# Kernel tuning notes

Measured on AMD Instinct MI355X. Metric: run time of the kernel, lower is better.

Reference implementation:

```python
import jax, jax.numpy as jnp
import numpy as np

N_NODES = 250000
N_EDGES = 4000000

def gcn_layer(x, src, dst, W, b, n_nodes):
    # PyG GCNConv: linear transform, add self-loops, symmetric normalization,
    # scatter-add aggregation at target nodes, then bias.
    xw = x @ W                                            # [N, out]
    deg = jax.ops.segment_sum(jnp.ones_like(src, dtype=xw.dtype), dst,
                              num_segments=n_nodes) + 1.0  # +1 for self loop
    dinv = deg ** -0.5                                     # deg >= 1 due to self loops
    norm = dinv[src] * dinv[dst]                           # [E]
    agg = jax.ops.segment_sum(norm[:, None] * xw[src], dst,
                              num_segments=n_nodes)        # neighbor messages
    out = agg + (dinv * dinv)[:, None] * xw + b            # self-loop message + bias
    return out


def setup_inputs() -> dict:
    key = jax.random.key(0)
    ks = jax.random.split(key, 8)
    x = jax.random.normal(ks[0], (N_NODES, 2), dtype=jnp.float32)
    edge_index = jax.random.randint(ks[1], (2, N_EDGES), 0, N_NODES, dtype=jnp.int64)
    def glorot(k, shape):
        lim = np.sqrt(6.0 / (shape[0] + shape[1]))
        return jax.random.uniform(k, shape, jnp.float32, -lim, lim)
    return {
        "x": x,
        "edge_index": edge_index,
        "W1": glorot(ks[2], (2, 16)),  "b1": jnp.zeros((16,), jnp.float32),
        "W2": glorot(ks[3], (16, 16)), "b2": jnp.zeros((16,), jnp.float32),
        "W3": glorot(ks[4], (16, 1)),  "b3": jnp.zeros((1,), jnp.float32),
    }


def reference(x, edge_index, W1, b1, W2, b2, W3, b3):
    src, dst = edge_index[0], edge_index[1]
    n = x.shape[0]
    h = jax.nn.relu(gcn_layer(x, src, dst, W1, b1, n))
    h = jax.nn.relu(gcn_layer(h, src, dst, W2, b2, n))
    return gcn_layer(h, src, dst, W3, b3, n)
```

## Files before the change

### kernel.cpp

```cpp
#include <hip/hip_runtime.h>


constexpr int NPW = 256;
constexpr int K   = 977;
constexpr int B   = K * 8;
constexpr int G   = 256;
constexpr int F   = 16;


__global__ __launch_bounds__(1024) void k_bcount(const int* __restrict__ src,
        const int* __restrict__ dst, int* __restrict__ bcount,
        int E, int chunk, int npg) {
    __shared__ int h[B];
    for (int k = threadIdx.x; k < B; k += 1024) h[k] = 0;
    __syncthreads();
    int beg = blockIdx.x * chunk, end = min(beg + chunk, E);
    for (int i = beg + threadIdx.x; i < end; i += 1024) {
        int s = __builtin_nontemporal_load(&src[i]);
        int d = __builtin_nontemporal_load(&dst[i]);
        atomicAdd(&h[(d >> 8) * 8 + s / npg], 1);
    }
    __syncthreads();
    for (int k = threadIdx.x; k < B; k += 1024)
        bcount[blockIdx.x * B + k] = h[k];
}

__global__ __launch_bounds__(256) void k_colsum(const int* __restrict__ bcount,
        int* __restrict__ tot) {
    int k = blockIdx.x * 256 + threadIdx.x;
    if (k >= B) return;
    int s = 0;
    for (int b = 0; b < G; ++b) s += bcount[b * B + k];
    tot[k] = s;
}

__global__ __launch_bounds__(1024) void k_binscan(const int* __restrict__ tot,
        int* __restrict__ colbase, int E) {
    __shared__ int cs[1024];
    int t = threadIdx.x;
    int v[8];
    int mytot = 0;
#pragma unroll
    for (int p = 0; p < 8; ++p) {
        int k = t * 8 + p;
        v[p] = (k < B) ? tot[k] : 0;
        mytot += v[p];
    }
    cs[t] = mytot;
    __syncthreads();
    for (int off = 1; off < 1024; off <<= 1) {
        int x = (t >= off) ? cs[t - off] : 0;
        __syncthreads();
        cs[t] += x;
        __syncthreads();
    }
    int run = cs[t] - mytot;
#pragma unroll
    for (int p = 0; p < 8; ++p) {
        int k = t * 8 + p;
        if (k < B) colbase[k] = run;
        run += v[p];
    }
    if (t == 1023) colbase[B] = E;
}

__global__ __launch_bounds__(256) void k_rebase(int* __restrict__ bcount,
        const int* __restrict__ colbase) {
    int k = blockIdx.x * 256 + threadIdx.x;
    if (k >= B) return;
    int run = colbase[k];
    for (int b = 0; b < G; ++b) {
        int t = bcount[b * B + k];
        bcount[b * B + k] = run;
        run += t;
    }
}

__global__ __launch_bounds__(1024) void k_bfill(const int* __restrict__ src,
        const int* __restrict__ dst, const int* __restrict__ base,
        int* __restrict__ ent, int E, int chunk, int npg) {
    __shared__ int cur[B];
    for (int k = threadIdx.x; k < B; k += 1024)
        cur[k] = base[blockIdx.x * B + k];
    __syncthreads();
    int beg = blockIdx.x * chunk, end = min(beg + chunk, E);
    for (int i = beg + threadIdx.x; i < end; i += 1024) {
        int s = __builtin_nontemporal_load(&src[i]);
        int d = __builtin_nontemporal_load(&dst[i]);
        int g = s / npg;
        int pos = atomicAdd(&cur[(d >> 8) * 8 + g], 1);
        ent[pos] = ((s - g * npg) << 8) | (d & 255);
    }
}


__global__ __launch_bounds__(256) void k_prep(const int* __restrict__ ent,
        const int* __restrict__ colbase, const float* __restrict__ x,
        float* __restrict__ dinv, float* __restrict__ dx, int n) {
    __shared__ int h[NPW];
    h[threadIdx.x] = 0;
    __syncthreads();
    int beg = colbase[blockIdx.x * 8], end = colbase[blockIdx.x * 8 + 8];
    for (int e = beg + threadIdx.x; e < end; e += 256)
        atomicAdd(&h[ent[e] & 255], 1);
    __syncthreads();
    int i = (blockIdx.x << 8) + threadIdx.x;
    if (i < n) {
        float di = rsqrtf((float)h[threadIdx.x] + 1.0f);
        dinv[i] = di;
        float2 xv = reinterpret_cast<const float2*>(x)[i];
        reinterpret_cast<float2*>(dx)[i] = make_float2(di * xv.x, di * xv.y);
    }
}


__global__ __launch_bounds__(512) void k_layer1(const int* __restrict__ ent,
        const int* __restrict__ colbase, const float* __restrict__ dinv,
        const float* __restrict__ dx, const float* __restrict__ W1,
        const float* __restrict__ b1, float* __restrict__ dh1, int n, int npg) {
    __shared__ float acc[NPW * 2];
    __shared__ float sW[32];
    __shared__ float sb[16];
    if (threadIdx.x < 32) sW[threadIdx.x] = W1[threadIdx.x];
    if (threadIdx.x >= 32 && threadIdx.x < 48) sb[threadIdx.x - 32] = b1[threadIdx.x - 32];
    for (int t = threadIdx.x; t < NPW * 2; t += 512) acc[t] = 0.0f;
    __syncthreads();
    for (int g = 0; g < 8; ++g) {
        int sbase = g * npg;
        int beg = colbase[blockIdx.x * 8 + g], end = colbase[blockIdx.x * 8 + g + 1];
        int e = beg + threadIdx.x;
        for (; e + 512 < end; e += 1024) {
            int v0 = ent[e], v1 = ent[e + 512];
            float2 a0 = reinterpret_cast<const float2*>(dx)[sbase + (v0 >> 8)];
            float2 a1 = reinterpret_cast<const float2*>(dx)[sbase + (v1 >> 8)];
            atomicAdd(&acc[(v0 & 255) * 2 + 0], a0.x);
            atomicAdd(&acc[(v0 & 255) * 2 + 1], a0.y);
            atomicAdd(&acc[(v1 & 255) * 2 + 0], a1.x);
            atomicAdd(&acc[(v1 & 255) * 2 + 1], a1.y);
        }
        if (e < end) {
            int v = ent[e];
            float2 a = reinterpret_cast<const float2*>(dx)[sbase + (v >> 8)];
            atomicAdd(&acc[(v & 255) * 2 + 0], a.x);
            atomicAdd(&acc[(v & 255) * 2 + 1], a.y);
        }
    }
    __syncthreads();
    int r = threadIdx.x;
    if (r < NPW) {
        int i = (blockIdx.x << 8) + r;
        if (i < n) {
            float di = dinv[i];
            float2 ds = reinterpret_cast<const float2*>(dx)[i];
            float a0 = di * (acc[r * 2 + 0] + ds.x);
            float a1 = di * (acc[r * 2 + 1] + ds.y);
            float4* orow = reinterpret_cast<float4*>(dh1 + (size_t)i * F);
#pragma unroll
            for (int q = 0; q < 4; ++q) {
                float4 o;
                o.x = di * fmaxf(a0 * sW[4*q+0] + a1 * sW[16 + 4*q+0] + sb[4*q+0], 0.0f);
                o.y = di * fmaxf(a0 * sW[4*q+1] + a1 * sW[16 + 4*q+1] + sb[4*q+1], 0.0f);
                o.z = di * fmaxf(a0 * sW[4*q+2] + a1 * sW[16 + 4*q+2] + sb[4*q+2], 0.0f);
                o.w = di * fmaxf(a0 * sW[4*q+3] + a1 * sW[16 + 4*q+3] + sb[4*q+3], 0.0f);
                orow[q] = o;
            }
        }
    }
}


__global__ __launch_bounds__(256) void k_l2s(const int* __restrict__ ent,
        const int* __restrict__ colbase, const float* __restrict__ dh1,
        float* __restrict__ agg16, int npg) {
    __shared__ float acc[NPW * 17];
    for (int t = threadIdx.x; t < NPW * 17; t += 256) acc[t] = 0.0f;
    __syncthreads();
    int c = blockIdx.x >> 3, g = blockIdx.x & 7;
    int sbase = g * npg;
    int beg = colbase[blockIdx.x], end = colbase[blockIdx.x + 1];
    int q4 = (threadIdx.x & 3) * 4;
    int e = beg + (threadIdx.x >> 2);
    for (; e + 64 < end; e += 128) {
        int v0 = ent[e], v1 = ent[e + 64];
        float4 r0 = *reinterpret_cast<const float4*>(dh1 + (size_t)(sbase + (v0 >> 8)) * F + q4);
        float4 r1 = *reinterpret_cast<const float4*>(dh1 + (size_t)(sbase + (v1 >> 8)) * F + q4);
        int a0 = (v0 & 255) * 17 + q4;
        int a1 = (v1 & 255) * 17 + q4;
        atomicAdd(&acc[a0 + 0], r0.x); atomicAdd(&acc[a0 + 1], r0.y);
        atomicAdd(&acc[a0 + 2], r0.z); atomicAdd(&acc[a0 + 3], r0.w);
        atomicAdd(&acc[a1 + 0], r1.x); atomicAdd(&acc[a1 + 1], r1.y);
        atomicAdd(&acc[a1 + 2], r1.z); atomicAdd(&acc[a1 + 3], r1.w);
    }
    if (e < end) {
        int v = ent[e];
        float4 r = *reinterpret_cast<const float4*>(dh1 + (size_t)(sbase + (v >> 8)) * F + q4);
        int a0 = (v & 255) * 17 + q4;
        atomicAdd(&acc[a0 + 0], r.x); atomicAdd(&acc[a0 + 1], r.y);
        atomicAdd(&acc[a0 + 2], r.z); atomicAdd(&acc[a0 + 3], r.w);
    }
    __syncthreads();
    float* aggc = agg16 + (size_t)c * NPW * F;
    for (int t = threadIdx.x; t < NPW * F; t += 256)
        atomicAdd(&aggc[t], acc[(t >> 4) * 17 + (t & 15)]);
}

__global__ __launch_bounds__(256) void k_l2b(const float* __restrict__ agg16,
        const float* __restrict__ dh1, const float* __restrict__ dinv,
        const float* __restrict__ W2, const float* __restrict__ b2,
        const float* __restrict__ W3, float* __restrict__ dxw3, int n) {
    __shared__ float sW2[256];
    __shared__ float sW3[16];
    __shared__ float sb[16];
    sW2[threadIdx.x] = W2[threadIdx.x];
    if (threadIdx.x < 16) sW3[threadIdx.x] = W3[threadIdx.x];
    else if (threadIdx.x < 32) sb[threadIdx.x - 16] = b2[threadIdx.x - 16];
    __syncthreads();
    int i = blockIdx.x * 256 + threadIdx.x;
    if (i >= n) return;
    float di = dinv[i];
    const float* ag = agg16 + (size_t)i * F;
    const float* dh = dh1 + (size_t)i * F;
    float a[16];
#pragma unroll
    for (int q = 0; q < 16; ++q) a[q] = di * (ag[q] + dh[q]);
    float sum = 0.0f;
#pragma unroll
    for (int c = 0; c < 16; ++c) {
        float h = sb[c];
#pragma unroll
        for (int q = 0; q < 16; ++q) h += a[q] * sW2[q * 16 + c];
        sum += fmaxf(h, 0.0f) * sW3[c];
    }
    dxw3[i] = di * sum;
}


__global__ __launch_bounds__(512) void k_out(const int* __restrict__ ent,
        const int* __restrict__ colbase, const float* __restrict__ dinv,
        const float* __restrict__ dxw3, const float* __restrict__ b3,
        float* __restrict__ out, int n, int npg) {
    __shared__ float acc[NPW];
    for (int t = threadIdx.x; t < NPW; t += 512) acc[t] = 0.0f;
    __syncthreads();
    for (int g = 0; g < 8; ++g) {
        int sbase = g * npg;
        int beg = colbase[blockIdx.x * 8 + g], end = colbase[blockIdx.x * 8 + g + 1];
        int e = beg + threadIdx.x;
        for (; e + 512 < end; e += 1024) {
            int v0 = ent[e], v1 = ent[e + 512];
            float s0 = dxw3[sbase + (v0 >> 8)];
            float s1 = dxw3[sbase + (v1 >> 8)];
            atomicAdd(&acc[v0 & 255], s0);
            atomicAdd(&acc[v1 & 255], s1);
        }
        if (e < end) {
            int v = ent[e];
            atomicAdd(&acc[v & 255], dxw3[sbase + (v >> 8)]);
        }
    }
    __syncthreads();
    int r = threadIdx.x;
    if (r < NPW) {
        int i = (blockIdx.x << 8) + r;
        if (i < n) out[i] = dinv[i] * (acc[r] + dxw3[i]) + b3[0];
    }
}


extern "C" void kernel_launch(void* const* d_in, const int* in_sizes, int n_in,
                              void* d_out, int out_size, void* d_ws, size_t ws_size,
                              hipStream_t stream) {
    const float* x  = (const float*)d_in[0];
    const int*   ei = (const int*)d_in[1];
    const float* W1 = (const float*)d_in[2];
    const float* b1 = (const float*)d_in[3];
    const float* W2 = (const float*)d_in[4];
    const float* b2 = (const float*)d_in[5];
    const float* W3 = (const float*)d_in[6];
    const float* b3 = (const float*)d_in[7];

    const int n = in_sizes[0] / 2;
    const int E = in_sizes[1] / 2;
    const int* src = ei;
    const int* dst = ei + E;
    const int npg = (n + 7) / 8;

    char* w = (char*)d_ws;
    int*   ent     = (int*)w;                 w += (size_t)E * 4;
    int*   bcount  = (int*)w;                 w += (size_t)G * B * 4;
    int*   tot     = (int*)w;                 w += (size_t)B * 4;
    int*   colbase = (int*)w;                 w += (size_t)(B + 1) * 4;
    w = (char*)(((uintptr_t)w + 15) & ~(uintptr_t)15);
    float* dinv    = (float*)w;               w += (size_t)n * 4;
    float* dx      = (float*)w;               w += (size_t)n * 2 * 4;
    float* dh1     = (float*)w;               w += (size_t)n * F * 4;
    float* agg16   = (float*)w;               w += (size_t)K * NPW * F * 4;
    float* dxw3    = (float*)w;               w += (size_t)n * 4;
    float* out     = (float*)d_out;

    const int chunk = (E + G - 1) / G;
    const int gridN = (n + 255) / 256;
    const int gridB = (B + 255) / 256;

    k_bcount <<<G, 1024, 0, stream>>>(src, dst, bcount, E, chunk, npg);
    k_colsum <<<gridB, 256, 0, stream>>>(bcount, tot);
    k_binscan<<<1, 1024, 0, stream>>>(tot, colbase, E);
    k_rebase <<<gridB, 256, 0, stream>>>(bcount, colbase);
    k_bfill  <<<G, 1024, 0, stream>>>(src, dst, bcount, ent, E, chunk, npg);

    k_prep<<<K, 256, 0, stream>>>(ent, colbase, x, dinv, dx, n);

    k_layer1<<<K, 512, 0, stream>>>(ent, colbase, dinv, dx, W1, b1, dh1, n, npg);

    hipMemsetAsync(agg16, 0, (size_t)K * NPW * F * 4, stream);
    k_l2s<<<B, 256, 0, stream>>>(ent, colbase, dh1, agg16, npg);
    k_l2b<<<gridN, 256, 0, stream>>>(agg16, dh1, dinv, W2, b2, W3, dxw3, n);

    k_out<<<K, 512, 0, stream>>>(ent, colbase, dinv, dxw3, b3, out, n, npg);
}
```

Measured before the change: 583.4 us.

## Fuse layer-2 scatter and dense transform into one per-column-block kernel

The layer-2 aggregation, previously split into 8 blocks per destination column that flushed partial sums to a global buffer with atomics, followed by a separate dense kernel, is merged into one kernel. Each block now walks all 8 source groups for its 256 destination nodes, keeps the full sum in LDS, then applies W2, ReLU and W3 directly. This removes the memset, the global atomic flush and the round trip through the agg16 buffer, plus one launch. In exchange there are 8x fewer blocks (977), each doing more serial work, which lowers parallelism and makes load balance depend more on per-block edge counts.

```diff
diff --git a/kernel.cpp b/kernel.cpp
--- a/kernel.cpp
+++ b/kernel.cpp
@@ -169,69 +169,66 @@
 }
 
 
-__global__ __launch_bounds__(256) void k_l2s(const int* __restrict__ ent,
-        const int* __restrict__ colbase, const float* __restrict__ dh1,
-        float* __restrict__ agg16, int npg) {
+__global__ __launch_bounds__(512) void k_layer2(const int* __restrict__ ent,
+        const int* __restrict__ colbase, const float* __restrict__ dinv,
+        const float* __restrict__ dh1, const float* __restrict__ W2,
+        const float* __restrict__ b2, const float* __restrict__ W3,
+        float* __restrict__ dxw3, int n, int npg) {
     __shared__ float acc[NPW * 17];
-    for (int t = threadIdx.x; t < NPW * 17; t += 256) acc[t] = 0.0f;
-    __syncthreads();
-    int c = blockIdx.x >> 3, g = blockIdx.x & 7;
-    int sbase = g * npg;
-    int beg = colbase[blockIdx.x], end = colbase[blockIdx.x + 1];
-    int q4 = (threadIdx.x & 3) * 4;
-    int e = beg + (threadIdx.x >> 2);
-    for (; e + 64 < end; e += 128) {
-        int v0 = ent[e], v1 = ent[e + 64];
-        float4 r0 = *reinterpret_cast<const float4*>(dh1 + (size_t)(sbase + (v0 >> 8)) * F + q4);
-        float4 r1 = *reinterpret_cast<const float4*>(dh1 + (size_t)(sbase + (v1 >> 8)) * F + q4);
-        int a0 = (v0 & 255) * 17 + q4;
-        int a1 = (v1 & 255) * 17 + q4;
-        atomicAdd(&acc[a0 + 0], r0.x); atomicAdd(&acc[a0 + 1], r0.y);
-        atomicAdd(&acc[a0 + 2], r0.z); atomicAdd(&acc[a0 + 3], r0.w);
-        atomicAdd(&acc[a1 + 0], r1.x); atomicAdd(&acc[a1 + 1], r1.y);
-        atomicAdd(&acc[a1 + 2], r1.z); atomicAdd(&acc[a1 + 3], r1.w);
-    }
-    if (e < end) {
-        int v = ent[e];
-        float4 r = *reinterpret_cast<const float4*>(dh1 + (size_t)(sbase + (v >> 8)) * F + q4);
-        int a0 = (v & 255) * 17 + q4;
-        atomicAdd(&acc[a0 + 0], r.x); atomicAdd(&acc[a0 + 1], r.y);
-        atomicAdd(&acc[a0 + 2], r.z); atomicAdd(&acc[a0 + 3], r.w);
-    }
-    __syncthreads();
-    float* aggc = agg16 + (size_t)c * NPW * F;
-    for (int t = threadIdx.x; t < NPW * F; t += 256)
-        atomicAdd(&aggc[t], acc[(t >> 4) * 17 + (t & 15)]);
-}
-
-__global__ __launch_bounds__(256) void k_l2b(const float* __restrict__ agg16,
-        const float* __restrict__ dh1, const float* __restrict__ dinv,
-        const float* __restrict__ W2, const float* __restrict__ b2,
-        const float* __restrict__ W3, float* __restrict__ dxw3, int n) {
     __shared__ float sW2[256];
     __shared__ float sW3[16];
     __shared__ float sb[16];
-    sW2[threadIdx.x] = W2[threadIdx.x];
-    if (threadIdx.x < 16) sW3[threadIdx.x] = W3[threadIdx.x];
-    else if (threadIdx.x < 32) sb[threadIdx.x - 16] = b2[threadIdx.x - 16];
-    __syncthreads();
-    int i = blockIdx.x * 256 + threadIdx.x;
-    if (i >= n) return;
-    float di = dinv[i];
-    const float* ag = agg16 + (size_t)i * F;
-    const float* dh = dh1 + (size_t)i * F;
-    float a[16];
-#pragma unroll
-    for (int q = 0; q < 16; ++q) a[q] = di * (ag[q] + dh[q]);
-    float sum = 0.0f;
-#pragma unroll
-    for (int c = 0; c < 16; ++c) {
-        float h = sb[c];
-#pragma unroll
-        for (int q = 0; q < 16; ++q) h += a[q] * sW2[q * 16 + c];
-        sum += fmaxf(h, 0.0f) * sW3[c];
-    }
-    dxw3[i] = di * sum;
+    if (threadIdx.x < 256) sW2[threadIdx.x] = W2[threadIdx.x];
+    else if (threadIdx.x < 272) sW3[threadIdx.x - 256] = W3[threadIdx.x - 256];
+    else if (threadIdx.x < 288) sb[threadIdx.x - 272] = b2[threadIdx.x - 272];
+    for (int t = threadIdx.x; t < NPW * 17; t += 512) acc[t] = 0.0f;
+    __syncthreads();
+    int q4 = (threadIdx.x & 3) * 4;
+    int slot = threadIdx.x >> 2;
+    for (int g = 0; g < 8; ++g) {
+        int sbase = g * npg;
+        int beg = colbase[blockIdx.x * 8 + g], end = colbase[blockIdx.x * 8 + g + 1];
+        int e = beg + slot;
+        for (; e + 128 < end; e += 256) {
+            int v0 = ent[e], v1 = ent[e + 128];
+            float4 r0 = *reinterpret_cast<const float4*>(dh1 + (size_t)(sbase + (v0 >> 8)) * F + q4);
+            float4 r1 = *reinterpret_cast<const float4*>(dh1 + (size_t)(sbase + (v1 >> 8)) * F + q4);
+            int a0 = (v0 & 255) * 17 + q4;
+            int a1 = (v1 & 255) * 17 + q4;
+            atomicAdd(&acc[a0 + 0], r0.x); atomicAdd(&acc[a0 + 1], r0.y);
+            atomicAdd(&acc[a0 + 2], r0.z); atomicAdd(&acc[a0 + 3], r0.w);
+            atomicAdd(&acc[a1 + 0], r1.x); atomicAdd(&acc[a1 + 1], r1.y);
+            atomicAdd(&acc[a1 + 2], r1.z); atomicAdd(&acc[a1 + 3], r1.w);
+        }
+        if (e < end) {
+            int v = ent[e];
+            float4 r = *reinterpret_cast<const float4*>(dh1 + (size_t)(sbase + (v >> 8)) * F + q4);
+            int a0 = (v & 255) * 17 + q4;
+            atomicAdd(&acc[a0 + 0], r.x); atomicAdd(&acc[a0 + 1], r.y);
+            atomicAdd(&acc[a0 + 2], r.z); atomicAdd(&acc[a0 + 3], r.w);
+        }
+    }
+    __syncthreads();
+    int r = threadIdx.x;
+    if (r < NPW) {
+        int i = (blockIdx.x << 8) + r;
+        if (i < n) {
+            float di = dinv[i];
+            const float* dh = dh1 + (size_t)i * F;
+            float a[16];
+#pragma unroll
+            for (int q = 0; q < 16; ++q) a[q] = di * (acc[r * 17 + q] + dh[q]);
+            float sum = 0.0f;
+#pragma unroll
+            for (int c = 0; c < 16; ++c) {
+                float h = sb[c];
+#pragma unroll
+                for (int q = 0; q < 16; ++q) h += a[q] * sW2[q * 16 + c];
+                sum += fmaxf(h, 0.0f) * sW3[c];
+            }
+            dxw3[i] = di * sum;
+        }
+    }
 }
 
 
@@ -294,12 +291,10 @@
     float* dinv    = (float*)w;               w += (size_t)n * 4;
     float* dx      = (float*)w;               w += (size_t)n * 2 * 4;
     float* dh1     = (float*)w;               w += (size_t)n * F * 4;
-    float* agg16   = (float*)w;               w += (size_t)K * NPW * F * 4;
     float* dxw3    = (float*)w;               w += (size_t)n * 4;
     float* out     = (float*)d_out;
 
     const int chunk = (E + G - 1) / G;
-    const int gridN = (n + 255) / 256;
     const int gridB = (B + 255) / 256;
 
     k_bcount <<<G, 1024, 0, stream>>>(src, dst, bcount, E, chunk, npg);
@@ -311,10 +306,6 @@
     k_prep<<<K, 256, 0, stream>>>(ent, colbase, x, dinv, dx, n);
 
     k_layer1<<<K, 512, 0, stream>>>(ent, colbase, dinv, dx, W1, b1, dh1, n, npg);
-
-    hipMemsetAsync(agg16, 0, (size_t)K * NPW * F * 4, stream);
-    k_l2s<<<B, 256, 0, stream>>>(ent, colbase, dh1, agg16, npg);
-    k_l2b<<<gridN, 256, 0, stream>>>(agg16, dh1, dinv, W2, b2, W3, dxw3, n);
-
-    k_out<<<K, 512, 0, stream>>>(ent, colbase, dinv, dxw3, b3, out, n, npg);
-}
+    k_layer2<<<K, 512, 0, stream>>>(ent, colbase, dinv, dh1, W2, b2, W3, dxw3, n, npg);
+    k_out   <<<K, 512, 0, stream>>>(ent, colbase, dinv, dxw3, b3, out, n, npg);
+}
```

Measured after the change: 572.0 us. No clear change (-1.9%).

## Replace global atomic aggregation with per-block partials and reduction; shrink binning grid

Applied to the files above, without the earlier changes.

Layer-2 scatter blocks now write their shared-memory partial sums with plain non-temporal stores into a per-block partial buffer. A new reduction kernel sums the 8 source-group partials per node chunk and then applies W2, ReLU and W3. This removes the memset and the global float atomics but adds about 128MB of partial traffic, and it falls back to the atomic path when workspace is too small. The binning kernels also drop from 256 to 32 blocks, which shrinks the bcount matrix and the column scans but lowers parallelism in count and fill.

```diff
diff --git a/kernel.cpp b/kernel.cpp
--- a/kernel.cpp
+++ b/kernel.cpp
@@ -4,7 +4,7 @@
 constexpr int NPW = 256;
 constexpr int K   = 977;
 constexpr int B   = K * 8;
-constexpr int G   = 256;
+constexpr int GB_ = 32;
 constexpr int F   = 16;
 
 
@@ -30,7 +30,7 @@
     int k = blockIdx.x * 256 + threadIdx.x;
     if (k >= B) return;
     int s = 0;
-    for (int b = 0; b < G; ++b) s += bcount[b * B + k];
+    for (int b = 0; b < GB_; ++b) s += bcount[b * B + k];
     tot[k] = s;
 }
 
@@ -69,7 +69,7 @@
     int k = blockIdx.x * 256 + threadIdx.x;
     if (k >= B) return;
     int run = colbase[k];
-    for (int b = 0; b < G; ++b) {
+    for (int b = 0; b < GB_; ++b) {
         int t = bcount[b * B + k];
         bcount[b * B + k] = run;
         run += t;
@@ -171,11 +171,11 @@
 
 __global__ __launch_bounds__(256) void k_l2s(const int* __restrict__ ent,
         const int* __restrict__ colbase, const float* __restrict__ dh1,
-        float* __restrict__ agg16, int npg) {
+        float* __restrict__ part, int npg) {
     __shared__ float acc[NPW * 17];
     for (int t = threadIdx.x; t < NPW * 17; t += 256) acc[t] = 0.0f;
     __syncthreads();
-    int c = blockIdx.x >> 3, g = blockIdx.x & 7;
+    int g = blockIdx.x & 7;
     int sbase = g * npg;
     int beg = colbase[blockIdx.x], end = colbase[blockIdx.x + 1];
     int q4 = (threadIdx.x & 3) * 4;
@@ -199,6 +199,75 @@
         atomicAdd(&acc[a0 + 2], r.z); atomicAdd(&acc[a0 + 3], r.w);
     }
     __syncthreads();
+    float* p = part + (size_t)blockIdx.x * (NPW * F);
+    for (int t = threadIdx.x; t < NPW * F; t += 256)
+        __builtin_nontemporal_store(acc[(t >> 4) * 17 + (t & 15)], &p[t]);
+}
+
+
+__global__ __launch_bounds__(256) void k_l2r(const float* __restrict__ part,
+        const float* __restrict__ dh1, const float* __restrict__ dinv,
+        const float* __restrict__ W2, const float* __restrict__ b2,
+        const float* __restrict__ W3, float* __restrict__ dxw3, int n) {
+    __shared__ float sW2[256];
+    __shared__ float sW3[16];
+    __shared__ float sb[16];
+    sW2[threadIdx.x] = W2[threadIdx.x];
+    if (threadIdx.x < 16) sW3[threadIdx.x] = W3[threadIdx.x];
+    else if (threadIdx.x < 32) sb[threadIdx.x - 16] = b2[threadIdx.x - 16];
+    __syncthreads();
+    int c = blockIdx.x, r = threadIdx.x;
+    int i = (c << 8) + r;
+    float a[16];
+#pragma unroll
+    for (int q = 0; q < 16; ++q) a[q] = 0.0f;
+    const float* pc = part + (size_t)c * 8 * (NPW * F) + r * F;
+#pragma unroll
+    for (int g = 0; g < 8; ++g) {
+        const float4* pg = reinterpret_cast<const float4*>(pc + (size_t)g * (NPW * F));
+#pragma unroll
+        for (int q = 0; q < 4; ++q) {
+            float4 v = pg[q];
+            a[4*q+0] += v.x; a[4*q+1] += v.y; a[4*q+2] += v.z; a[4*q+3] += v.w;
+        }
+    }
+    if (i < n) {
+        float di = dinv[i];
+        const float* dh = dh1 + (size_t)i * F;
+#pragma unroll
+        for (int q = 0; q < 16; ++q) a[q] = di * (a[q] + dh[q]);
+        float sum = 0.0f;
+#pragma unroll
+        for (int cc = 0; cc < 16; ++cc) {
+            float h = sb[cc];
+#pragma unroll
+            for (int q = 0; q < 16; ++q) h += a[q] * sW2[q * 16 + cc];
+            sum += fmaxf(h, 0.0f) * sW3[cc];
+        }
+        dxw3[i] = di * sum;
+    }
+}
+
+
+__global__ __launch_bounds__(256) void k_l2s_at(const int* __restrict__ ent,
+        const int* __restrict__ colbase, const float* __restrict__ dh1,
+        float* __restrict__ agg16, int npg) {
+    __shared__ float acc[NPW * 17];
+    for (int t = threadIdx.x; t < NPW * 17; t += 256) acc[t] = 0.0f;
+    __syncthreads();
+    int c = blockIdx.x >> 3, g = blockIdx.x & 7;
+    int sbase = g * npg;
+    int beg = colbase[blockIdx.x], end = colbase[blockIdx.x + 1];
+    int q4 = (threadIdx.x & 3) * 4;
+    int e = beg + (threadIdx.x >> 2);
+    for (; e < end; e += 64) {
+        int v = ent[e];
+        float4 r = *reinterpret_cast<const float4*>(dh1 + (size_t)(sbase + (v >> 8)) * F + q4);
+        int a0 = (v & 255) * 17 + q4;
+        atomicAdd(&acc[a0 + 0], r.x); atomicAdd(&acc[a0 + 1], r.y);
+        atomicAdd(&acc[a0 + 2], r.z); atomicAdd(&acc[a0 + 3], r.w);
+    }
+    __syncthreads();
     float* aggc = agg16 + (size_t)c * NPW * F;
     for (int t = threadIdx.x; t < NPW * F; t += 256)
         atomicAdd(&aggc[t], acc[(t >> 4) * 17 + (t & 15)]);
@@ -225,11 +294,11 @@
     for (int q = 0; q < 16; ++q) a[q] = di * (ag[q] + dh[q]);
     float sum = 0.0f;
 #pragma unroll
-    for (int c = 0; c < 16; ++c) {
-        float h = sb[c];
-#pragma unroll
-        for (int q = 0; q < 16; ++q) h += a[q] * sW2[q * 16 + c];
-        sum += fmaxf(h, 0.0f) * sW3[c];
+    for (int cc = 0; cc < 16; ++cc) {
+        float h = sb[cc];
+#pragma unroll
+        for (int q = 0; q < 16; ++q) h += a[q] * sW2[q * 16 + cc];
+        sum += fmaxf(h, 0.0f) * sW3[cc];
     }
     dxw3[i] = di * sum;
 }
@@ -285,36 +354,44 @@
     const int* dst = ei + E;
     const int npg = (n + 7) / 8;
 
-    char* w = (char*)d_ws;
+    char* w0 = (char*)d_ws;
+    char* w = w0;
     int*   ent     = (int*)w;                 w += (size_t)E * 4;
-    int*   bcount  = (int*)w;                 w += (size_t)G * B * 4;
+    int*   bcount  = (int*)w;                 w += (size_t)GB_ * B * 4;
     int*   tot     = (int*)w;                 w += (size_t)B * 4;
     int*   colbase = (int*)w;                 w += (size_t)(B + 1) * 4;
     w = (char*)(((uintptr_t)w + 15) & ~(uintptr_t)15);
     float* dinv    = (float*)w;               w += (size_t)n * 4;
     float* dx      = (float*)w;               w += (size_t)n * 2 * 4;
     float* dh1     = (float*)w;               w += (size_t)n * F * 4;
-    float* agg16   = (float*)w;               w += (size_t)K * NPW * F * 4;
     float* dxw3    = (float*)w;               w += (size_t)n * 4;
+    float* part    = (float*)w;
+    size_t need_part = (size_t)(w - w0) + (size_t)B * NPW * F * 4;
     float* out     = (float*)d_out;
 
-    const int chunk = (E + G - 1) / G;
+    const int chunk = (E + GB_ - 1) / GB_;
+    const int gridB = (B + 255) / 256;
     const int gridN = (n + 255) / 256;
-    const int gridB = (B + 255) / 256;
-
-    k_bcount <<<G, 1024, 0, stream>>>(src, dst, bcount, E, chunk, npg);
+
+    k_bcount <<<GB_, 1024, 0, stream>>>(src, dst, bcount, E, chunk, npg);
     k_colsum <<<gridB, 256, 0, stream>>>(bcount, tot);
     k_binscan<<<1, 1024, 0, stream>>>(tot, colbase, E);
     k_rebase <<<gridB, 256, 0, stream>>>(bcount, colbase);
-    k_bfill  <<<G, 1024, 0, stream>>>(src, dst, bcount, ent, E, chunk, npg);
+    k_bfill  <<<GB_, 1024, 0, stream>>>(src, dst, bcount, ent, E, chunk, npg);
 
     k_prep<<<K, 256, 0, stream>>>(ent, colbase, x, dinv, dx, n);
 
     k_layer1<<<K, 512, 0, stream>>>(ent, colbase, dinv, dx, W1, b1, dh1, n, npg);
 
-    hipMemsetAsync(agg16, 0, (size_t)K * NPW * F * 4, stream);
-    k_l2s<<<B, 256, 0, stream>>>(ent, colbase, dh1, agg16, npg);
-    k_l2b<<<gridN, 256, 0, stream>>>(agg16, dh1, dinv, W2, b2, W3, dxw3, n);
+    if (ws_size >= need_part) {
+        k_l2s<<<B, 256, 0, stream>>>(ent, colbase, dh1, part, npg);
+        k_l2r<<<K, 256, 0, stream>>>(part, dh1, dinv, W2, b2, W3, dxw3, n);
+    } else {
+        float* agg16 = part;
+        (void)hipMemsetAsync(agg16, 0, (size_t)K * NPW * F * 4, stream);
+        k_l2s_at<<<B, 256, 0, stream>>>(ent, colbase, dh1, agg16, npg);
+        k_l2b<<<gridN, 256, 0, stream>>>(agg16, dh1, dinv, W2, b2, W3, dxw3, n);
+    }
 
     k_out<<<K, 512, 0, stream>>>(ent, colbase, dinv, dxw3, b3, out, n, npg);
 }
```

New measurement: 834.9 us. 1.43x slower.
